# Kernel tuning notes

Hardware: AMD Instinct MI355X
Metric: run time of the kernel (lower is better)

## Reference

```python
import jax, jax.numpy as jnp
import numpy as np
from jax import lax

D, H, V = 640, 1760, 50257
B, S = 8, 512
SCALE = 0.02


def _lstm_layer(x, w_ih, w_hh, b_ih, b_hh):
    # x: [B,S,in], weights: [4H,in],[4H,H]; PyTorch gate order i,f,g,o
    Hh = w_hh.shape[1]
    xg = jnp.einsum('bsd,gd->bsg', x, w_ih) + b_ih + b_hh  # [B,S,4H]
    xg_t = jnp.swapaxes(xg, 0, 1)  # [S,B,4H]
    h0 = jnp.zeros((x.shape[0], Hh), x.dtype)
    c0 = jnp.zeros((x.shape[0], Hh), x.dtype)

    def step(carry, g_t):
        h, c = carry
        g = g_t + h @ w_hh.T
        i, f, gg, o = jnp.split(g, 4, axis=-1)
        c = jax.nn.sigmoid(f) * c + jax.nn.sigmoid(i) * jnp.tanh(gg)
        h = jax.nn.sigmoid(o) * jnp.tanh(c)
        return (h, c), h

    _, hs = lax.scan(step, (h0, c0), xg_t)
    return jnp.swapaxes(hs, 0, 1)  # [B,S,H]


def setup_inputs() -> dict:
    key = jax.random.key(0)
    ks = jax.random.split(key, 16)
    ids = jax.random.randint(ks[0], (B, S), 0, V)
    inp = {'ids': ids,
           'emb': jax.random.normal(ks[1], (V, D), jnp.float32) * SCALE}
    kidx = 2
    for l, din in enumerate([D, H, H]):
        inp[f'w_ih_{l}'] = jax.random.normal(ks[kidx], (4 * H, din), jnp.float32) * SCALE; kidx += 1
        inp[f'w_hh_{l}'] = jax.random.normal(ks[kidx], (4 * H, H), jnp.float32) * SCALE; kidx += 1
        b = jnp.zeros((4 * H,), jnp.float32).at[H:2 * H].set(1.0)  # forget bias = 1
        inp[f'b_ih_{l}'] = b
        inp[f'b_hh_{l}'] = jnp.zeros((4 * H,), jnp.float32)
    inp['ln_g'] = jnp.ones((H,), jnp.float32)
    inp['ln_b'] = jnp.zeros((H,), jnp.float32)
    inp['proj_w'] = jax.random.normal(ks[kidx], (D, H), jnp.float32) * SCALE
    return inp


def reference(ids, emb, w_ih_0, w_hh_0, b_ih_0, b_hh_0,
              w_ih_1, w_hh_1, b_ih_1, b_hh_1,
              w_ih_2, w_hh_2, b_ih_2, b_hh_2,
              ln_g, ln_b, proj_w):
    x = emb[ids]  # [B,S,D]
    x = _lstm_layer(x, w_ih_0, w_hh_0, b_ih_0, b_hh_0)
    x = _lstm_layer(x, w_ih_1, w_hh_1, b_ih_1, b_hh_1)
    x = _lstm_layer(x, w_ih_2, w_hh_2, b_ih_2, b_hh_2)
    # LayerNorm over H
    mu = jnp.mean(x, axis=-1, keepdims=True)
    var = jnp.var(x, axis=-1, keepdims=True)
    x = (x - mu) * lax.rsqrt(var + 1e-5) * ln_g + ln_b
    x = jnp.einsum('bsh,dh->bsd', x, proj_w)  # proj to d_model
    return jnp.einsum('bsd,vd->bsv', x, emb)  # tied head logits
```

## Files before the change

kernel.cpp:

```cpp
#include <hip/hip_runtime.h>
#include <hip/hip_bf16.h>

#define DMODEL 640
#define HDIM   1760
#define G4     7040
#define VOCAB  50257
#define VPAD   50304
#define SEQ    512
#define MROWS  4096
#define NWG    220
#define NCNT   8
#define WSTRIDE 1800

typedef __attribute__((ext_vector_type(8))) short short8_t;
typedef __attribute__((ext_vector_type(4))) short s16x4;
typedef __attribute__((ext_vector_type(4))) float f32x4;

static __device__ __forceinline__ float bf2f(short s) {
  union { unsigned int u; float f; } v;
  v.u = ((unsigned int)(unsigned short)s) << 16;
  return v.f;
}
static __device__ __forceinline__ short f2bf(float f) {
  union { float f; unsigned int u; } v; v.f = f;
  unsigned int r = v.u + 0x7fffu + ((v.u >> 16) & 1u);
  return (short)(r >> 16);
}

static __device__ __forceinline__ short8_t ld16_coh(const short* p) {
  short8_t r;
  asm volatile("global_load_dwordx4 %0, %1, off sc0 sc1" : "=v"(r) : "v"(p));
  return r;
}
static __device__ __forceinline__ void st8_coh(short* p, s16x4 v) {
  asm volatile("global_store_dwordx2 %0, %1, off sc0 sc1" :: "v"(p), "v"(v) : "memory");
}

__global__ void cvt_f32_bf16(const float* __restrict__ src, short* __restrict__ dst, long n) {
  long i = ((long)blockIdx.x * blockDim.x + threadIdx.x) * 8;
  if (i + 8 <= n) {
    float4 a = *(const float4*)(src + i);
    float4 b = *(const float4*)(src + i + 4);
    short8_t o;
    o[0] = f2bf(a.x); o[1] = f2bf(a.y); o[2] = f2bf(a.z); o[3] = f2bf(a.w);
    o[4] = f2bf(b.x); o[5] = f2bf(b.y); o[6] = f2bf(b.z); o[7] = f2bf(b.w);
    *(short8_t*)(dst + i) = o;
  } else {
    for (; i < n; ++i) dst[i] = f2bf(src[i]);
  }
}

__global__ void embed_gather(const int* __restrict__ ids, const float* __restrict__ emb,
                             short* __restrict__ x0) {
  int row = blockIdx.x;
  int id  = ids[row];
  const float* s = emb + (long)id * DMODEL;
  short* d = x0 + (long)row * DMODEL;
  for (int c = threadIdx.x; c < DMODEL; c += blockDim.x) d[c] = f2bf(s[c]);
}

#define GLDS16(gp, lp) __builtin_amdgcn_global_load_lds( \
    (const __attribute__((address_space(1))) unsigned int*)(gp), \
    (__attribute__((address_space(3))) unsigned int*)(lp), 16, 0, 0)

template<int OUT_BF16>
__global__ __launch_bounds__(256, 2) void gemm_btn(
    const short* __restrict__ A, const short* __restrict__ B, void* __restrict__ C,
    int M, int N, int K)
{
  __shared__ short As[128 * 32];
  __shared__ short Bs[128 * 32];
  const int bn = blockIdx.x * 128, bm = blockIdx.y * 128;
  const int tid = threadIdx.x, lane = tid & 63, wid = tid >> 6;
  const int wm = (wid >> 1) * 64, wn = (wid & 1) * 64;

  f32x4 acc[4][4] = {};

  const int c0 = 2 * wid;
  const int srow = c0 * 16 + (lane >> 2);
  const int scol = (lane & 3) * 8;
  const long aoff0 = (long)(bm + srow) * K + scol;
  const long aoff1 = aoff0 + 16 * (long)K;
  const long boff0 = (long)(bn + srow) * K + scol;
  const long boff1 = boff0 + 16 * (long)K;
  short* Asw0 = As + c0 * 512; short* Asw1 = Asw0 + 512;
  short* Bsw0 = Bs + c0 * 512; short* Bsw1 = Bsw0 + 512;

  for (int bk = 0; bk < K; bk += 32) {
    GLDS16(A + aoff0 + bk, Asw0);
    GLDS16(A + aoff1 + bk, Asw1);
    GLDS16(B + boff0 + bk, Bsw0);
    GLDS16(B + boff1 + bk, Bsw1);
    __syncthreads();
    short8_t af[4], bfr[4];
#pragma unroll
    for (int m = 0; m < 4; ++m)
      af[m] = *(const short8_t*)&As[(wm + m * 16 + (lane & 15)) * 32 + (lane >> 4) * 8];
#pragma unroll
    for (int n = 0; n < 4; ++n)
      bfr[n] = *(const short8_t*)&Bs[(wn + n * 16 + (lane & 15)) * 32 + (lane >> 4) * 8];
#pragma unroll
    for (int m = 0; m < 4; ++m)
#pragma unroll
      for (int n = 0; n < 4; ++n)
        acc[m][n] = __builtin_amdgcn_mfma_f32_16x16x32_bf16(af[m], bfr[n], acc[m][n], 0, 0, 0);
    __syncthreads();
  }

#pragma unroll
  for (int m = 0; m < 4; ++m) {
#pragma unroll
    for (int n = 0; n < 4; ++n) {
      int col = bn + wn + n * 16 + (lane & 15);
      if (col < N) {
        int rbase = bm + wm + m * 16 + (lane >> 4) * 4;
#pragma unroll
        for (int i = 0; i < 4; ++i) {
          long idx = (long)(rbase + i) * N + col;
          if (OUT_BF16) ((short*)C)[idx] = f2bf(acc[m][n][i]);
          else          ((float*)C)[idx] = acc[m][n][i];
        }
      }
    }
  }
}

__global__ __launch_bounds__(256, 1) void lstm_scan(
    const short* __restrict__ whh,
    const short* __restrict__ xg,
    const float* __restrict__ bih, const float* __restrict__ bhh,
    short* __restrict__ xout,
    int* __restrict__ sync, int layer)
{
  __shared__ short Ws[32][WSTRIDE];
  __shared__ float red[4][2][64][4];

  const int wg = blockIdx.x, tid = threadIdx.x, lane = tid & 63, wid = tid >> 6;
  const int j0 = wg * 8;

  for (int c = tid; c < 32 * 448; c += 256) {
    int r = c / 448, cc = (c % 448) * 4;
    s16x4 v = {0, 0, 0, 0};
    if (cc < HDIM) {
      int grow = (r >> 3) * HDIM + j0 + (r & 7);
      v = *(const s16x4*)&whh[(long)grow * HDIM + cc];
    }
    *(s16x4*)&Ws[r][cc] = v;
  }

  const int b = lane & 15;
  const int jrel = (lane >> 4) * 4;
  const bool active = (wid == 0) && (lane < 32) && (b < 8);

  float bI[4], bF[4], bG[4], bO[4];
  float cst[4] = {0.f, 0.f, 0.f, 0.f};
  if (active) {
#pragma unroll
    for (int i = 0; i < 4; ++i) {
      int j = j0 + jrel + i;
      bI[i] = bih[j]            + bhh[j];
      bF[i] = bih[HDIM + j]     + bhh[HDIM + j];
      bG[i] = bih[2 * HDIM + j] + bhh[2 * HDIM + j];
      bO[i] = bih[3 * HDIM + j] + bhh[3 * HDIM + j];
    }
  }

  const int ks0 = wid * 14;
  const int bc = (b < 7) ? b : 7;
  const long hlane = (long)(bc * SEQ) * HDIM + (lane >> 4) * 8;
  const int awrow0 = lane & 15, awrow1 = 16 + (lane & 15);
  const int acol = (lane >> 4) * 8;

  int* cnts = sync;
  int* gof  = sync + 256;

  __syncthreads();

  for (int t = 0; t < SEQ; ++t) {
    s16x4 xi, xf, xgg, xo;
    if (active) {
      const short* xrow = xg + (long)(b * SEQ + t) * G4;
      xi  = *(const s16x4*)(xrow + j0 + jrel);
      xf  = *(const s16x4*)(xrow + HDIM + j0 + jrel);
      xgg = *(const s16x4*)(xrow + 2 * HDIM + j0 + jrel);
      xo  = *(const s16x4*)(xrow + 3 * HDIM + j0 + jrel);
    }

    f32x4 acc0 = {0.f, 0.f, 0.f, 0.f}, acc1 = {0.f, 0.f, 0.f, 0.f};
    if (t > 0) {
      const short* hb = xout + hlane + (long)(t - 1) * HDIM;
      short8_t hreg[14];
#pragma unroll
      for (int kkl = 0; kkl < 14; ++kkl)
        hreg[kkl] = ld16_coh(hb + (ks0 + kkl) * 32);
      asm volatile("s_waitcnt vmcnt(0)" ::: "memory");
      __builtin_amdgcn_sched_barrier(0);
#pragma unroll
      for (int kkl = 0; kkl < 14; ++kkl) {
        int kc = (ks0 + kkl) * 32 + acol;
        short8_t a0 = *(const short8_t*)&Ws[awrow0][kc];
        short8_t a1 = *(const short8_t*)&Ws[awrow1][kc];
        acc0 = __builtin_amdgcn_mfma_f32_16x16x32_bf16(a0, hreg[kkl], acc0, 0, 0, 0);
        acc1 = __builtin_amdgcn_mfma_f32_16x16x32_bf16(a1, hreg[kkl], acc1, 0, 0, 0);
      }
    }
    *(f32x4*)&red[wid][0][lane][0] = acc0;
    *(f32x4*)&red[wid][1][lane][0] = acc1;
    __syncthreads();

    if (wid == 0) {
#pragma unroll
      for (int w = 1; w < 4; ++w) {
        acc0 += *(const f32x4*)&red[w][0][lane][0];
        acc1 += *(const f32x4*)&red[w][1][lane][0];
      }
      f32x4 fac, oac;
#pragma unroll
      for (int i = 0; i < 4; ++i) {
        fac[i] = __shfl_xor(acc0[i], 32);
        oac[i] = __shfl_xor(acc1[i], 32);
      }
      if (active) {
        s16x4 hv;
#pragma unroll
        for (int i = 0; i < 4; ++i) {
          float pi = acc0[i] + bf2f(xi[i])  + bI[i];
          float pf = fac[i]  + bf2f(xf[i])  + bF[i];
          float pg = acc1[i] + bf2f(xgg[i]) + bG[i];
          float po = oac[i]  + bf2f(xo[i])  + bO[i];
          float ig = 1.f / (1.f + __expf(-pi));
          float fg = 1.f / (1.f + __expf(-pf));
          float og = 1.f / (1.f + __expf(-po));
          float gg = tanhf(pg);
          cst[i] = fg * cst[i] + ig * gg;
          hv[i] = f2bf(og * tanhf(cst[i]));
        }
        st8_coh(xout + (long)(b * SEQ + t) * HDIM + j0 + jrel, hv);
      }
      asm volatile("s_waitcnt vmcnt(0)" ::: "memory");
    }
    __syncthreads();

    if (tid == 0) {
      const int gstep = layer * SEQ + t + 1;
      __hip_atomic_fetch_add(&cnts[(wg & (NCNT - 1)) * 32], 1,
                             __ATOMIC_RELAXED, __HIP_MEMORY_SCOPE_AGENT);
      if (t < SEQ - 1) {
        if (wg == 0) {
          const int target = NWG * gstep;
          int s;
          do {
            s = 0;
#pragma unroll
            for (int c = 0; c < NCNT; ++c)
              s += __hip_atomic_load(&cnts[c * 32], __ATOMIC_RELAXED, __HIP_MEMORY_SCOPE_AGENT);
          } while (s < target);
          __hip_atomic_store(gof, gstep, __ATOMIC_RELAXED, __HIP_MEMORY_SCOPE_AGENT);
        } else {
          while (__hip_atomic_load(gof, __ATOMIC_RELAXED, __HIP_MEMORY_SCOPE_AGENT) < gstep)
            __builtin_amdgcn_s_sleep(1);
        }
      }
    }
    __syncthreads();
  }
}

__global__ __launch_bounds__(256) void ln_fwd(
    const short* __restrict__ x, const float* __restrict__ g, const float* __restrict__ bb,
    short* __restrict__ y)
{
  __shared__ float rs[8];
  const int row = blockIdx.x, tid = threadIdx.x;
  const short* xr = x + (long)row * HDIM;
  float s1 = 0.f, s2 = 0.f;
  for (int c = tid; c < HDIM; c += 256) { float f = bf2f(xr[c]); s1 += f; s2 += f * f; }
  for (int off = 32; off; off >>= 1) { s1 += __shfl_xor(s1, off); s2 += __shfl_xor(s2, off); }
  if ((tid & 63) == 0) { rs[(tid >> 6) * 2] = s1; rs[(tid >> 6) * 2 + 1] = s2; }
  __syncthreads();
  s1 = rs[0] + rs[2] + rs[4] + rs[6];
  s2 = rs[1] + rs[3] + rs[5] + rs[7];
  const float mu = s1 / HDIM;
  const float rstd = rsqrtf(s2 / HDIM - mu * mu + 1e-5f);
  for (int c = tid; c < HDIM; c += 256) {
    float f = bf2f(xr[c]);
    y[(long)row * HDIM + c] = f2bf((f - mu) * rstd * g[c] + bb[c]);
  }
}

extern "C" void kernel_launch(void* const* d_in, const int* in_sizes, int n_in,
                              void* d_out, int out_size, void* d_ws, size_t ws_size,
                              hipStream_t stream) {
  (void)in_sizes; (void)n_in; (void)out_size; (void)ws_size;
  const int*   ids  = (const int*)d_in[0];
  const float* emb  = (const float*)d_in[1];
  const float* wih[3] = {(const float*)d_in[2], (const float*)d_in[6], (const float*)d_in[10]};
  const float* whh[3] = {(const float*)d_in[3], (const float*)d_in[7], (const float*)d_in[11]};
  const float* bih[3] = {(const float*)d_in[4], (const float*)d_in[8], (const float*)d_in[12]};
  const float* bhh[3] = {(const float*)d_in[5], (const float*)d_in[9], (const float*)d_in[13]};
  const float* lng  = (const float*)d_in[14];
  const float* lnb  = (const float*)d_in[15];
  const float* prjw = (const float*)d_in[16];
  float* out = (float*)d_out;

  char* p = (char*)d_ws;
  auto alloc = [&](size_t bytes) { char* r = p; p += (bytes + 255) & ~(size_t)255; return r; };
  short* emb_b = (short*)alloc((size_t)VPAD * DMODEL * 2);
  short* wbuf  = (short*)alloc((size_t)G4 * HDIM * 2);
  short* xgbuf = (short*)alloc((size_t)MROWS * G4 * 2);
  short* x0    = (short*)alloc((size_t)MROWS * DMODEL * 2);
  short* xb1   = (short*)alloc((size_t)MROWS * HDIM * 2);
  short* xb2   = (short*)alloc((size_t)MROWS * HDIM * 2);
  short* pbuf  = (short*)alloc((size_t)MROWS * DMODEL * 2);
  int*   sync  = (int*)alloc(4096);

  hipMemsetAsync(sync, 0, 4096, stream);

  auto cvt = [&](const float* s, short* d, long n) {
    int blocks = (int)((n / 8 + 255) / 256);
    cvt_f32_bf16<<<dim3(blocks), dim3(256), 0, stream>>>(s, d, n);
  };

  cvt(emb, emb_b, (long)VOCAB * DMODEL);
  embed_gather<<<dim3(MROWS), dim3(256), 0, stream>>>(ids, emb, x0);

  short* xin = x0; int kin = DMODEL;
  short* xouts[3] = {xb1, xb2, xb1};
  for (int l = 0; l < 3; ++l) {
    cvt(wih[l], wbuf, (long)G4 * kin);
    gemm_btn<1><<<dim3(G4 / 128, MROWS / 128), dim3(256), 0, stream>>>(
        xin, wbuf, (void*)xgbuf, MROWS, G4, kin);
    cvt(whh[l], wbuf, (long)G4 * HDIM);
    lstm_scan<<<dim3(NWG), dim3(256), 0, stream>>>(
        wbuf, xgbuf, bih[l], bhh[l], xouts[l], sync, l);
    xin = xouts[l]; kin = HDIM;
  }

  ln_fwd<<<dim3(MROWS), dim3(256), 0, stream>>>(xb1, lng, lnb, xb2);
  cvt(prjw, wbuf, (long)DMODEL * HDIM);
  gemm_btn<1><<<dim3(DMODEL / 128, MROWS / 128), dim3(256), 0, stream>>>(
      xb2, wbuf, (void*)pbuf, MROWS, DMODEL, HDIM);
  gemm_btn<0><<<dim3((VOCAB + 127) / 128, MROWS / 128), dim3(256), 0, stream>>>(
      pbuf, emb_b, (void*)out, MROWS, VOCAB, DMODEL);
}
```

Baseline: 8.670 ms.

## Replace grid barrier in LSTM scan with poison-value dataflow polling

Drops the per-timestep global atomic counter barrier across all 220 workgroups. Each output buffer is pre-filled with a NaN poison pattern, and consumers re-load the previous hidden state until none of their words match the poison. A third hidden-state buffer is added so no layer reuses poisoned memory, and a fill kernel runs before the layers. This removes barrier latency but risks false stalls if a real bf16 pair equals the poison value, and it relies on coherent loads and stores to order the data.

```diff
diff --git a/kernel.cpp b/kernel.cpp
--- a/kernel.cpp
+++ b/kernel.cpp
@@ -9,8 +9,8 @@
 #define SEQ    512
 #define MROWS  4096
 #define NWG    220
-#define NCNT   8
 #define WSTRIDE 1800
+#define POIS   0x7FC07FC0u
 
 typedef __attribute__((ext_vector_type(8))) short short8_t;
 typedef __attribute__((ext_vector_type(4))) short s16x4;
@@ -27,13 +27,21 @@
   return (short)(r >> 16);
 }
 
-static __device__ __forceinline__ short8_t ld16_coh(const short* p) {
-  short8_t r;
+static __device__ __forceinline__ uint4 ld16_coh(const short* p) {
+  uint4 r;
   asm volatile("global_load_dwordx4 %0, %1, off sc0 sc1" : "=v"(r) : "v"(p));
   return r;
 }
 static __device__ __forceinline__ void st8_coh(short* p, s16x4 v) {
   asm volatile("global_store_dwordx2 %0, %1, off sc0 sc1" :: "v"(p), "v"(v) : "memory");
+}
+
+__global__ void fill_poison(unsigned int* __restrict__ dst, long n4) {
+  long i = (long)blockIdx.x * blockDim.x + threadIdx.x;
+  if (i < n4) {
+    uint4 v = {POIS, POIS, POIS, POIS};
+    *(uint4*)(dst + i * 4) = v;
+  }
 }
 
 __global__ void cvt_f32_bf16(const float* __restrict__ src, short* __restrict__ dst, long n) {
@@ -129,8 +137,7 @@
     const short* __restrict__ whh,
     const short* __restrict__ xg,
     const float* __restrict__ bih, const float* __restrict__ bhh,
-    short* __restrict__ xout,
-    int* __restrict__ sync, int layer)
+    short* __restrict__ xout)
 {
   __shared__ short Ws[32][WSTRIDE];
   __shared__ float red[4][2][64][4];
@@ -170,9 +177,6 @@
   const long hlane = (long)(bc * SEQ) * HDIM + (lane >> 4) * 8;
   const int awrow0 = lane & 15, awrow1 = 16 + (lane & 15);
   const int acol = (lane >> 4) * 8;
-
-  int* cnts = sync;
-  int* gof  = sync + 256;
 
   __syncthreads();
 
@@ -189,19 +193,39 @@
     f32x4 acc0 = {0.f, 0.f, 0.f, 0.f}, acc1 = {0.f, 0.f, 0.f, 0.f};
     if (t > 0) {
       const short* hb = xout + hlane + (long)(t - 1) * HDIM;
-      short8_t hreg[14];
-#pragma unroll
-      for (int kkl = 0; kkl < 14; ++kkl)
-        hreg[kkl] = ld16_coh(hb + (ks0 + kkl) * 32);
-      asm volatile("s_waitcnt vmcnt(0)" ::: "memory");
+      uint4 hreg[14];
+#pragma unroll
+      for (int k = 0; k < 14; ++k) {
+        if (ks0 + k < 55) hreg[k] = ld16_coh(hb + (ks0 + k) * 32);
+        else              hreg[k] = (uint4){0u, 0u, 0u, 0u};
+      }
+      for (;;) {
+        asm volatile("s_waitcnt vmcnt(0)" ::: "memory");
+        __builtin_amdgcn_sched_barrier(0);
+        unsigned bad = 0;
+#pragma unroll
+        for (int k = 0; k < 14; ++k) {
+          if (ks0 + k < 55) {
+            bool p = (hreg[k].x == POIS) | (hreg[k].y == POIS) |
+                     (hreg[k].z == POIS) | (hreg[k].w == POIS);
+            bad |= p ? (1u << k) : 0u;
+          }
+        }
+        if (!__any((int)(bad != 0u))) break;
+#pragma unroll
+        for (int k = 0; k < 14; ++k)
+          if ((ks0 + k < 55) && (bad & (1u << k)))
+            hreg[k] = ld16_coh(hb + (ks0 + k) * 32);
+      }
       __builtin_amdgcn_sched_barrier(0);
 #pragma unroll
-      for (int kkl = 0; kkl < 14; ++kkl) {
-        int kc = (ks0 + kkl) * 32 + acol;
+      for (int k = 0; k < 14; ++k) {
+        int kc = (ks0 + k) * 32 + acol;
+        short8_t hv = __builtin_bit_cast(short8_t, hreg[k]);
         short8_t a0 = *(const short8_t*)&Ws[awrow0][kc];
         short8_t a1 = *(const short8_t*)&Ws[awrow1][kc];
-        acc0 = __builtin_amdgcn_mfma_f32_16x16x32_bf16(a0, hreg[kkl], acc0, 0, 0, 0);
-        acc1 = __builtin_amdgcn_mfma_f32_16x16x32_bf16(a1, hreg[kkl], acc1, 0, 0, 0);
+        acc0 = __builtin_amdgcn_mfma_f32_16x16x32_bf16(a0, hv, acc0, 0, 0, 0);
+        acc1 = __builtin_amdgcn_mfma_f32_16x16x32_bf16(a1, hv, acc1, 0, 0, 0);
       }
     }
     *(f32x4*)&red[wid][0][lane][0] = acc0;
@@ -236,30 +260,6 @@
           hv[i] = f2bf(og * tanhf(cst[i]));
         }
         st8_coh(xout + (long)(b * SEQ + t) * HDIM + j0 + jrel, hv);
-      }
-      asm volatile("s_waitcnt vmcnt(0)" ::: "memory");
-    }
-    __syncthreads();
-
-    if (tid == 0) {
-      const int gstep = layer * SEQ + t + 1;
-      __hip_atomic_fetch_add(&cnts[(wg & (NCNT - 1)) * 32], 1,
-                             __ATOMIC_RELAXED, __HIP_MEMORY_SCOPE_AGENT);
-      if (t < SEQ - 1) {
-        if (wg == 0) {
-          const int target = NWG * gstep;
-          int s;
-          do {
-            s = 0;
-#pragma unroll
-            for (int c = 0; c < NCNT; ++c)
-              s += __hip_atomic_load(&cnts[c * 32], __ATOMIC_RELAXED, __HIP_MEMORY_SCOPE_AGENT);
-          } while (s < target);
-          __hip_atomic_store(gof, gstep, __ATOMIC_RELAXED, __HIP_MEMORY_SCOPE_AGENT);
-        } else {
-          while (__hip_atomic_load(gof, __ATOMIC_RELAXED, __HIP_MEMORY_SCOPE_AGENT) < gstep)
-            __builtin_amdgcn_s_sleep(1);
-        }
       }
     }
     __syncthreads();
@@ -311,10 +311,14 @@
   short* x0    = (short*)alloc((size_t)MROWS * DMODEL * 2);
   short* xb1   = (short*)alloc((size_t)MROWS * HDIM * 2);
   short* xb2   = (short*)alloc((size_t)MROWS * HDIM * 2);
+  short* xb3   = (short*)alloc((size_t)MROWS * HDIM * 2);
   short* pbuf  = (short*)alloc((size_t)MROWS * DMODEL * 2);
-  int*   sync  = (int*)alloc(4096);
-
-  hipMemsetAsync(sync, 0, 4096, stream);
+
+  {
+    long n4 = (long)3 * MROWS * HDIM / 8;
+    fill_poison<<<dim3((unsigned)((n4 + 255) / 256)), dim3(256), 0, stream>>>(
+        (unsigned int*)xb1, n4);
+  }
 
   auto cvt = [&](const float* s, short* d, long n) {
     int blocks = (int)((n / 8 + 255) / 256);
@@ -325,18 +329,18 @@
   embed_gather<<<dim3(MROWS), dim3(256), 0, stream>>>(ids, emb, x0);
 
   short* xin = x0; int kin = DMODEL;
-  short* xouts[3] = {xb1, xb2, xb1};
+  short* xouts[3] = {xb1, xb2, xb3};
   for (int l = 0; l < 3; ++l) {
     cvt(wih[l], wbuf, (long)G4 * kin);
     gemm_btn<1><<<dim3(G4 / 128, MROWS / 128), dim3(256), 0, stream>>>(
         xin, wbuf, (void*)xgbuf, MROWS, G4, kin);
     cvt(whh[l], wbuf, (long)G4 * HDIM);
     lstm_scan<<<dim3(NWG), dim3(256), 0, stream>>>(
-        wbuf, xgbuf, bih[l], bhh[l], xouts[l], sync, l);
+        wbuf, xgbuf, bih[l], bhh[l], xouts[l]);
     xin = xouts[l]; kin = HDIM;
   }
 
-  ln_fwd<<<dim3(MROWS), dim3(256), 0, stream>>>(xb1, lng, lnb, xb2);
+  ln_fwd<<<dim3(MROWS), dim3(256), 0, stream>>>(xb3, lng, lnb, xb2);
   cvt(prjw, wbuf, (long)DMODEL * HDIM);
   gemm_btn<1><<<dim3(DMODEL / 128, MROWS / 128), dim3(256), 0, stream>>>(
       xb2, wbuf, (void*)pbuf, MROWS, DMODEL, HDIM);
```

Result: slower. 11.00 ms (+26.8%).

## Replace centralized grid barrier with distributed per-wave counter polling

Applied to the files above, without the earlier changes.

Removes the master-workgroup barrier (wg 0 sums counters, then publishes a flag for the others to poll) and the two block-wide __syncthreads per step. Each wave now polls 32 striped counters directly with coherent loads and a wave reduction before reading h(t-1), and increments its workgroup's counter after storing its h slice. This cuts one hop of global-memory latency from every recurrent step. Layer 2 now writes to a separate third buffer, because other workgroups may still be reading layer 1 output while it runs. The cost is more polling traffic from many waves at once, plus reliance on relaxed atomics for ordering.

```diff
diff --git a/kernel.cpp b/kernel.cpp
--- a/kernel.cpp
+++ b/kernel.cpp
@@ -9,7 +9,7 @@
 #define SEQ    512
 #define MROWS  4096
 #define NWG    220
-#define NCNT   8
+#define NCNT   32
 #define WSTRIDE 1800
 
 typedef __attribute__((ext_vector_type(8))) short short8_t;
@@ -30,6 +30,11 @@
 static __device__ __forceinline__ short8_t ld16_coh(const short* p) {
   short8_t r;
   asm volatile("global_load_dwordx4 %0, %1, off sc0 sc1" : "=v"(r) : "v"(p));
+  return r;
+}
+static __device__ __forceinline__ int ld4_coh(const int* p) {
+  int r;
+  asm volatile("global_load_dword %0, %1, off sc0 sc1" : "=v"(r) : "v"(p));
   return r;
 }
 static __device__ __forceinline__ void st8_coh(short* p, s16x4 v) {
@@ -172,7 +177,7 @@
   const int acol = (lane >> 4) * 8;
 
   int* cnts = sync;
-  int* gof  = sync + 256;
+  int* mycnt = &cnts[(lane & 31) * 32];
 
   __syncthreads();
 
@@ -188,20 +193,32 @@
 
     f32x4 acc0 = {0.f, 0.f, 0.f, 0.f}, acc1 = {0.f, 0.f, 0.f, 0.f};
     if (t > 0) {
+      const int target = NWG * (layer * SEQ + t);
+      int total;
+      do {
+        int v = 0;
+        if (lane < 32) v = ld4_coh(mycnt);
+        asm volatile("s_waitcnt vmcnt(0)" ::: "memory");
+        int s = v;
+#pragma unroll
+        for (int off = 1; off < 32; off <<= 1) s += __shfl_xor(s, off);
+        total = s + __shfl_xor(s, 32);
+      } while (total < target);
+
       const short* hb = xout + hlane + (long)(t - 1) * HDIM;
       short8_t hreg[14];
 #pragma unroll
-      for (int kkl = 0; kkl < 14; ++kkl)
-        hreg[kkl] = ld16_coh(hb + (ks0 + kkl) * 32);
+      for (int k = 0; k < 14; ++k)
+        hreg[k] = ld16_coh(hb + (ks0 + k) * 32);
       asm volatile("s_waitcnt vmcnt(0)" ::: "memory");
       __builtin_amdgcn_sched_barrier(0);
 #pragma unroll
-      for (int kkl = 0; kkl < 14; ++kkl) {
-        int kc = (ks0 + kkl) * 32 + acol;
+      for (int k = 0; k < 14; ++k) {
+        int kc = (ks0 + k) * 32 + acol;
         short8_t a0 = *(const short8_t*)&Ws[awrow0][kc];
         short8_t a1 = *(const short8_t*)&Ws[awrow1][kc];
-        acc0 = __builtin_amdgcn_mfma_f32_16x16x32_bf16(a0, hreg[kkl], acc0, 0, 0, 0);
-        acc1 = __builtin_amdgcn_mfma_f32_16x16x32_bf16(a1, hreg[kkl], acc1, 0, 0, 0);
+        acc0 = __builtin_amdgcn_mfma_f32_16x16x32_bf16(a0, hreg[k], acc0, 0, 0, 0);
+        acc1 = __builtin_amdgcn_mfma_f32_16x16x32_bf16(a1, hreg[k], acc1, 0, 0, 0);
       }
     }
     *(f32x4*)&red[wid][0][lane][0] = acc0;
@@ -238,31 +255,10 @@
         st8_coh(xout + (long)(b * SEQ + t) * HDIM + j0 + jrel, hv);
       }
       asm volatile("s_waitcnt vmcnt(0)" ::: "memory");
-    }
-    __syncthreads();
-
-    if (tid == 0) {
-      const int gstep = layer * SEQ + t + 1;
-      __hip_atomic_fetch_add(&cnts[(wg & (NCNT - 1)) * 32], 1,
-                             __ATOMIC_RELAXED, __HIP_MEMORY_SCOPE_AGENT);
-      if (t < SEQ - 1) {
-        if (wg == 0) {
-          const int target = NWG * gstep;
-          int s;
-          do {
-            s = 0;
-#pragma unroll
-            for (int c = 0; c < NCNT; ++c)
-              s += __hip_atomic_load(&cnts[c * 32], __ATOMIC_RELAXED, __HIP_MEMORY_SCOPE_AGENT);
-          } while (s < target);
-          __hip_atomic_store(gof, gstep, __ATOMIC_RELAXED, __HIP_MEMORY_SCOPE_AGENT);
-        } else {
-          while (__hip_atomic_load(gof, __ATOMIC_RELAXED, __HIP_MEMORY_SCOPE_AGENT) < gstep)
-            __builtin_amdgcn_s_sleep(1);
-        }
-      }
-    }
-    __syncthreads();
+      if (lane == 0)
+        __hip_atomic_fetch_add(&cnts[(wg & (NCNT - 1)) * 32], 1,
+                               __ATOMIC_RELAXED, __HIP_MEMORY_SCOPE_AGENT);
+    }
   }
 }
 
@@ -311,6 +307,7 @@
   short* x0    = (short*)alloc((size_t)MROWS * DMODEL * 2);
   short* xb1   = (short*)alloc((size_t)MROWS * HDIM * 2);
   short* xb2   = (short*)alloc((size_t)MROWS * HDIM * 2);
+  short* xb3   = (short*)alloc((size_t)MROWS * HDIM * 2);
   short* pbuf  = (short*)alloc((size_t)MROWS * DMODEL * 2);
   int*   sync  = (int*)alloc(4096);
 
@@ -325,7 +322,7 @@
   embed_gather<<<dim3(MROWS), dim3(256), 0, stream>>>(ids, emb, x0);
 
   short* xin = x0; int kin = DMODEL;
-  short* xouts[3] = {xb1, xb2, xb1};
+  short* xouts[3] = {xb1, xb2, xb3};
   for (int l = 0; l < 3; ++l) {
     cvt(wih[l], wbuf, (long)G4 * kin);
     gemm_btn<1><<<dim3(G4 / 128, MROWS / 128), dim3(256), 0, stream>>>(
@@ -336,7 +333,7 @@
     xin = xouts[l]; kin = HDIM;
   }
 
-  ln_fwd<<<dim3(MROWS), dim3(256), 0, stream>>>(xb1, lng, lnb, xb2);
+  ln_fwd<<<dim3(MROWS), dim3(256), 0, stream>>>(xb3, lng, lnb, xb2);
   cvt(prjw, wbuf, (long)DMODEL * HDIM);
   gemm_btn<1><<<dim3(DMODEL / 128, MROWS / 128), dim3(256), 0, stream>>>(
       xb2, wbuf, (void*)pbuf, MROWS, DMODEL, HDIM);
```

After: 9.208 ms. +6.2%, slower.
